# Performance work log

Hardware: AMD Instinct MI355X
Metric: run time of the kernel (lower is better)

The kernel has to match this reference:

```python
import jax, jax.numpy as jnp
import numpy as np

B, N, D, E = 16, 64, 512, 512
MSG = 512          # message_size must equal edge_feature_size (scatter into edge states)
LINK_H = 512       # GraphConv hidden channels
P = 2              # propagate_layers
HOI, ROLES = 26, 2


def setup_inputs() -> dict:
    key = jax.random.key(0)
    ks = jax.random.split(key, 12)
    s = 0.02
    return dict(
        edge_features=jax.random.normal(ks[0], (B, N, N, E), jnp.float32),
        node_features=jax.random.normal(ks[1], (B, N, D), jnp.float32),
        node_labels=jnp.zeros((B, N, HOI), jnp.float32),
        node_roles=jnp.zeros((B, N, ROLES), jnp.float32),
        # message_fun 'linear_concat_relu': Linear(D+E -> MSG) + ReLU
        Wm=(jax.random.normal(ks[2], (MSG, D + E), jnp.float32) * s),
        bm=jnp.zeros((MSG,), jnp.float32),
        # link_fun GraphConv: 1x1 Conv2d stack E->LINK_H->LINK_H->1
        Wl1=(jax.random.normal(ks[3], (LINK_H, E), jnp.float32) * s),
        bl1=jnp.zeros((LINK_H,), jnp.float32),
        Wl2=(jax.random.normal(ks[4], (LINK_H, LINK_H), jnp.float32) * s),
        bl2=jnp.zeros((LINK_H,), jnp.float32),
        Wlo=(jax.random.normal(ks[5], (1, LINK_H), jnp.float32) * s),
        blo=jnp.zeros((1,), jnp.float32),
        # update_fun GRU(input=MSG, hidden=D), torch gate order r,z,n
        W_ih=(jax.random.normal(ks[6], (3 * D, MSG), jnp.float32) * s),
        b_ih=jnp.zeros((3 * D,), jnp.float32),
        W_hh=(jax.random.normal(ks[7], (3 * D, D), jnp.float32) * s),
        b_hh=jnp.zeros((3 * D,), jnp.float32),
        # readout FCs
        Wr1=(jax.random.normal(ks[8], (HOI, D), jnp.float32) * s),
        br1=jnp.zeros((HOI,), jnp.float32),
        Wr2=(jax.random.normal(ks[9], (ROLES, D), jnp.float32) * s),
        br2=jnp.zeros((ROLES,), jnp.float32),
    )


def _link(x, Wl1, bl1, Wl2, bl2, Wlo, blo):
    # x: [B, C, N, N]; 1x1 conv stack -> [B, N, N]
    h = jax.nn.relu(jnp.einsum('bcvw,hc->bhvw', x, Wl1) + bl1[None, :, None, None])
    h = jax.nn.relu(jnp.einsum('bcvw,hc->bhvw', h, Wl2) + bl2[None, :, None, None])
    return (jnp.einsum('bcvw,hc->bhvw', h, Wlo) + blo[None, :, None, None])[:, 0]


def _forward(edge_features, node_features, Wm, bm, Wl1, bl1, Wl2, bl2, Wlo, blo,
             W_ih, b_ih, W_hh, b_hh, Wr1, br1, Wr2, br2):
    e = jnp.transpose(edge_features, (0, 3, 1, 2))   # [B,E,v,w]
    nf = jnp.transpose(node_features, (0, 2, 1))     # [B,D,N]
    # hidden node states are never written back in the source, so raw messages
    # m(h_w, e_vw) are constant across propagation rounds: compute once, vectorized over v.
    h_part = jnp.broadcast_to(nf[:, :, None, :], (B, D, N, N))   # h_w broadcast over v
    cat = jnp.concatenate([h_part, e], axis=1)                   # [B, D+E, v, w]
    M = jax.nn.relu(jnp.einsum('bcvw,mc->bmvw', cat, Wm) + bm[None, :, None, None])
    edge_state = e
    gated = M
    for _ in range(P):
        pred_adj = _link(edge_state, Wl1, bl1, Wl2, bl2, Wlo, blo)      # [B,v,w]
        gated = jax.nn.sigmoid(pred_adj)[:, None, :, :] * M            # [B,m,v,w]
        # source stores m_v into hidden_edge_states[..., :, :, i_node] (column v)
        edge_state = jnp.swapaxes(gated, 2, 3)
    m_sum = jnp.sum(gated, axis=3)                   # [B, m, v]
    x = jnp.swapaxes(m_sum, 1, 2)                    # [B, N, MSG] GRU input
    h = node_features                                # [B, N, D]  GRU hidden
    gi = x @ W_ih.T + b_ih
    gh = h @ W_hh.T + b_hh
    ir, iz, inn = jnp.split(gi, 3, axis=-1)
    hr, hz, hn = jnp.split(gh, 3, axis=-1)
    r = jax.nn.sigmoid(ir + hr)
    z = jax.nn.sigmoid(iz + hz)
    n = jnp.tanh(inn + r * hn)
    h_new = (1.0 - z) * n + z * h
    pred_node_labels = h_new @ Wr1.T + br1
    pred_node_roles = h_new @ Wr2.T + br2
    return pred_adj, pred_node_labels, pred_node_roles


def reference(edge_features, node_features, node_labels, node_roles, Wm, bm,
              Wl1, bl1, Wl2, bl2, Wlo, blo, W_ih, b_ih, W_hh, b_hh,
              Wr1, br1, Wr2, br2):
    return _forward(edge_features, node_features, Wm, bm, Wl1, bl1, Wl2, bl2,
                    Wlo, blo, W_ih, b_ih, W_hh, b_hh, Wr1, br1, Wr2, br2)
```

## Files before the change

kernel.cpp:

```cpp
#include <hip/hip_runtime.h>
#include <stdint.h>
#include <stddef.h>


using u16 = unsigned short;
using u32 = unsigned int;

__device__ __forceinline__ float u2f(u16 u) {
  union { unsigned i; float f; } c; c.i = ((unsigned)u) << 16; return c.f;
}
__device__ __forceinline__ u16 f2u(float f) {
  union { float f; unsigned i; } c; c.f = f;
  unsigned u = c.i;
  u += 0x7fffu + ((u >> 16) & 1u);
  return (u16)(u >> 16);
}
__device__ __forceinline__ u32 pk2(float lo, float hi) {
  return (u32)f2u(lo) | ((u32)f2u(hi) << 16);
}
__device__ __forceinline__ float sigm(float x) { return 1.f / (1.f + expf(-x)); }

typedef __attribute__((ext_vector_type(8))) short bfrag;
typedef __attribute__((ext_vector_type(4))) float f32x4;

__device__ __forceinline__ void gl_lds16(const u16* g, u16* l) {
  __builtin_amdgcn_global_load_lds((const __attribute__((address_space(1))) void*)g,
                                   (__attribute__((address_space(3))) void*)l,
                                   16, 0, 0);
}

#define NSEG 17
struct CvtArgs {
  const float* src[NSEG];
  u16* dst[NSEG];
  int cum[NSEG + 1];
};
__global__ __launch_bounds__(256) void cvt_multi(CvtArgs a, int total) {
  int i = blockIdx.x * 256 + threadIdx.x;
  if (i >= total) return;
  int s = 0;
  while (s + 1 < NSEG && i >= a.cum[s + 1]) ++s;
  const int off = i - a.cum[s];
  a.dst[s][off] = f2u(a.src[s][off]);
}

template <int MODE, bool A32>
__global__ __launch_bounds__(256)
void gemm_bt(const void* __restrict__ Av, int lda, size_t abase,
             const u16* __restrict__ W, int ldw, int K,
             const u16* __restrict__ bias,
             const float* __restrict__ ubuf,
             const u16* __restrict__ wlo,
             float* __restrict__ pred,
             u16* __restrict__ outb,
             float* __restrict__ outf,
             int ldc,
             const u16* __restrict__ W2, int ldw2, u16* __restrict__ outb2)
{
  __shared__ u16 smem[17408];
  constexpr int ASTR = A32 ? 72 : 64;
  u16* As = smem;
  u16* Bs = smem + (A32 ? 9216 : 8192);

  const int tid  = threadIdx.x;
  const int wave = tid >> 6, lane = tid & 63;
  const int wr = wave >> 1, wc = wave & 1;
  const int quad = lane >> 4, l16 = lane & 15;
  const int srow8 = lane >> 3;
  const int scol8 = (lane & 7) * 8;
  const int scolsw = ((lane & 7) ^ srow8) * 8;

  const int gx = gridDim.x;
  const int nwg = gx * gridDim.y;
  int flat = blockIdx.y * gx + blockIdx.x;
  if ((nwg & 7) == 0) { const int q = nwg >> 3; flat = (flat & 7) * q + (flat >> 3); }
  const int bx = flat % gx;
  const int by = flat / gx;

  const int row0 = by * 128;
  const bool isM = (MODE != 5) || (bx < 4);
  const int col0 = (MODE == 5 ? (bx & 3) : bx) * 128;
  const u16* Wp  = (MODE == 5 && !isM) ? W2  : W;
  const int ldwp = (MODE == 5 && !isM) ? ldw2 : ldw;

  f32x4 acc[4][4];
#pragma unroll
  for (int i = 0; i < 4; i++)
#pragma unroll
    for (int j = 0; j < 4; j++)
#pragma unroll
      for (int r = 0; r < 4; r++) acc[i][j][r] = 0.f;

  float4 rf[8];
  uint4  ra[4];
  if constexpr (A32) {
#pragma unroll
    for (int i = 0; i < 4; i++) {
      const int idx = i * 256 + tid, sr = idx >> 3, sc = (idx & 7) * 8;
      const float* p = (const float*)Av + (abase + (size_t)(row0 + sr)) * lda + sc;
      rf[2 * i] = *(const float4*)p;
      rf[2 * i + 1] = *(const float4*)(p + 4);
    }
#pragma unroll
    for (int i = 0; i < 4; i++) {
      ra[i].x = pk2(rf[2 * i].x, rf[2 * i].y);
      ra[i].y = pk2(rf[2 * i].z, rf[2 * i].w);
      ra[i].z = pk2(rf[2 * i + 1].x, rf[2 * i + 1].y);
      ra[i].w = pk2(rf[2 * i + 1].z, rf[2 * i + 1].w);
    }
  }

  for (int k0 = 0; k0 < K; k0 += 64) {
    __syncthreads();
    if constexpr (A32) {
#pragma unroll
      for (int i = 0; i < 4; i++) {
        const int idx = i * 256 + tid, sr = idx >> 3, sc = (idx & 7) * 8;
        *(uint4*)(As + sr * ASTR + sc) = ra[i];
      }
    } else {
#pragma unroll
      for (int i = 0; i < 4; i++) {
        const int chunk = wave * 4 + i;
        gl_lds16((const u16*)Av + (abase + (size_t)(row0 + chunk * 8 + srow8)) * lda + k0 + scolsw,
                 As + chunk * 512 + lane * 8);
      }
    }
#pragma unroll
    for (int i = 0; i < 4; i++) {
      const int chunk = wave * 4 + i;
      gl_lds16(Wp + (size_t)(col0 + chunk * 8 + srow8) * ldwp + k0 + scolsw,
               Bs + chunk * 512 + lane * 8);
    }
    __syncthreads();

    const bool more = (k0 + 64 < K);
    if constexpr (A32) {
      if (more) {
#pragma unroll
        for (int i = 0; i < 4; i++) {
          const int idx = i * 256 + tid, sr = idx >> 3, sc = (idx & 7) * 8;
          const float* p = (const float*)Av + (abase + (size_t)(row0 + sr)) * lda + (k0 + 64) + sc;
          rf[2 * i] = *(const float4*)p;
          rf[2 * i + 1] = *(const float4*)(p + 4);
        }
      }
    }

#pragma unroll
    for (int kk = 0; kk < 64; kk += 32) {
      const int cbsw = (((kk >> 3) + quad) ^ (l16 & 7)) << 3;
      bfrag af[4], bf[4];
#pragma unroll
      for (int mt = 0; mt < 4; mt++) {
        const int R = wr * 64 + mt * 16 + l16;
        if constexpr (A32)
          af[mt] = *(const bfrag*)(As + R * ASTR + kk + quad * 8);
        else
          af[mt] = *(const bfrag*)(As + R * 64 + cbsw);
      }
#pragma unroll
      for (int nt = 0; nt < 4; nt++) {
        const int R = wc * 64 + nt * 16 + l16;
        bf[nt] = *(const bfrag*)(Bs + R * 64 + cbsw);
      }
#pragma unroll
      for (int mt = 0; mt < 4; mt++)
#pragma unroll
        for (int nt = 0; nt < 4; nt++)
          acc[mt][nt] = __builtin_amdgcn_mfma_f32_16x16x32_bf16(af[mt], bf[nt], acc[mt][nt], 0, 0, 0);
    }

    if constexpr (A32) {
      if (more) {
#pragma unroll
        for (int i = 0; i < 4; i++) {
          ra[i].x = pk2(rf[2 * i].x, rf[2 * i].y);
          ra[i].y = pk2(rf[2 * i].z, rf[2 * i].w);
          ra[i].z = pk2(rf[2 * i + 1].x, rf[2 * i + 1].y);
          ra[i].w = pk2(rf[2 * i + 1].z, rf[2 * i + 1].w);
        }
      }
    }
  }

  if constexpr (MODE == 2) {
#pragma unroll
    for (int mt = 0; mt < 4; mt++) {
#pragma unroll
      for (int r = 0; r < 4; r++) {
        const int rg = row0 + wr * 64 + mt * 16 + quad * 4 + r;
        float s = 0.f;
#pragma unroll
        for (int nt = 0; nt < 4; nt++) {
          const int cg = col0 + wc * 64 + nt * 16 + l16;
          float v = acc[mt][nt][r] + u2f(bias[cg]);
          v = fmaxf(v, 0.f);
          s += v * u2f(wlo[cg]);
        }
#pragma unroll
        for (int off = 1; off < 16; off <<= 1) s += __shfl_xor(s, off, 16);
        if (l16 == 0) atomicAdd(pred + rg, s);
      }
    }
  } else if constexpr (MODE == 3) {
#pragma unroll
    for (int mt = 0; mt < 4; mt++)
#pragma unroll
      for (int nt = 0; nt < 4; nt++)
#pragma unroll
        for (int r = 0; r < 4; r++) {
          const int rg = row0 + wr * 64 + mt * 16 + quad * 4 + r;
          const int cg = col0 + wc * 64 + nt * 16 + l16;
          outf[(size_t)rg * ldc + cg] = acc[mt][nt][r] + u2f(bias[cg]);
        }
  } else {
    u16* tile = smem;
    u16* outp = (MODE == 5 && !isM) ? outb2 : outb;
    __syncthreads();
#pragma unroll
    for (int mt = 0; mt < 4; mt++)
#pragma unroll
      for (int nt = 0; nt < 4; nt++)
#pragma unroll
        for (int r = 0; r < 4; r++) {
          const int lrow = wr * 64 + mt * 16 + quad * 4 + r;
          const int lcol = wc * 64 + nt * 16 + l16;
          const int rg = row0 + lrow;
          const int cg = col0 + lcol;
          float v = acc[mt][nt][r];
          if (MODE == 0 || (MODE == 5 && isM)) {
            const size_t grow = abase + rg;
            const int urow = (int)(((grow >> 12) << 6) | (grow & 63));
            v += ubuf[(size_t)urow * 512 + cg];
            v = fmaxf(v, 0.f);
          } else if (MODE == 1 || MODE == 5) {
            v += u2f(bias[cg]);
            v = fmaxf(v, 0.f);
          } else {
            v = sigm(pred[rg]) * v + u2f(bias[cg]);
            v = fmaxf(v, 0.f);
          }
          tile[lrow * 136 + lcol] = f2u(v);
        }
    __syncthreads();
    const int row = tid >> 1, half = tid & 1;
    const u16* src = tile + row * 136 + half * 64;
    u16* dst = outp + (size_t)(row0 + row) * ldc + col0 + half * 64;
#pragma unroll
    for (int j = 0; j < 8; j++)
      *(uint4*)(dst + j * 8) = *(const uint4*)(src + j * 8);
  }
}

__global__ void fill_kernel(float* __restrict__ p, const u16* __restrict__ val, int n) {
  int i = blockIdx.x * blockDim.x + threadIdx.x;
  if (i < n) p[i] = u2f(*val);
}

__global__ void adj_out_kernel(const float* __restrict__ r, float* __restrict__ out) {
  int i = blockIdx.x * 256 + threadIdx.x;
  int b = i >> 12, v = (i >> 6) & 63, w = i & 63;
  out[i] = r[(b << 12) + (w << 6) + v];
}

__global__ __launch_bounds__(512)
void msum_kernel(const float* __restrict__ r, const u16* __restrict__ M, u16* __restrict__ x) {
  const int bv = blockIdx.x;
  const int b = bv >> 6, v = bv & 63;
  __shared__ float s[64];
  if (threadIdx.x < 64) {
    const int w = threadIdx.x;
    s[w] = sigm(r[(b << 12) + (w << 6) + v]);
  }
  __syncthreads();
  const int m = threadIdx.x;
  const u16* Mp = M + (((size_t)(b << 12) + (v << 6)) << 9) + m;
  float acc = 0.f;
#pragma unroll 8
  for (int w = 0; w < 64; w++) acc += s[w] * u2f(Mp[(size_t)w << 9]);
  x[(size_t)bv * 512 + m] = f2u(acc);
}

__global__ __launch_bounds__(256)
void gru_kernel(const float* __restrict__ gi, const float* __restrict__ gh,
                const u16* __restrict__ h, float* __restrict__ hn) {
  int i = blockIdx.x * 256 + threadIdx.x;
  int row = i >> 9, d = i & 511;
  const float* gir = gi + (size_t)row * 1536;
  const float* ghr = gh + (size_t)row * 1536;
  float rr = sigm(gir[d] + ghr[d]);
  float z  = sigm(gir[512 + d] + ghr[512 + d]);
  float n  = tanhf(gir[1024 + d] + rr * ghr[1024 + d]);
  float hv = u2f(h[i]);
  hn[i] = (1.f - z) * n + z * hv;
}

__global__ __launch_bounds__(256)
void readout_kernel(const float* __restrict__ hn,
                    const u16* __restrict__ Wr1, const u16* __restrict__ br1,
                    const u16* __restrict__ Wr2, const u16* __restrict__ br2,
                    float* __restrict__ out) {
  const int row = blockIdx.x;
  __shared__ float hrow[512];
  for (int d = threadIdx.x; d < 512; d += 256) hrow[d] = hn[(size_t)row * 512 + d];
  __syncthreads();
  const int wave = threadIdx.x >> 6, lane = threadIdx.x & 63;
  for (int j = wave; j < 28; j += 4) {
    const u16* wrow;
    float bias;
    size_t off;
    if (j < 26) { wrow = Wr1 + (size_t)j * 512; bias = u2f(br1[j]); off = 65536 + (size_t)row * 26 + j; }
    else { int jj = j - 26; wrow = Wr2 + (size_t)jj * 512; bias = u2f(br2[jj]); off = 92160 + (size_t)row * 2 + jj; }
    float s = 0.f;
    for (int d = lane; d < 512; d += 64) s += hrow[d] * u2f(wrow[d]);
#pragma unroll
    for (int o = 32; o; o >>= 1) s += __shfl_down(s, o);
    if (lane == 0) out[off] = s + bias;
  }
}

extern "C" void kernel_launch(void* const* d_in, const int* in_sizes, int n_in,
                              void* d_out, int out_size, void* d_ws, size_t ws_size,
                              hipStream_t stream)
{
  (void)in_sizes; (void)n_in; (void)out_size;
  const void*  X  = d_in[0];
  char* ws = (char*)d_ws;

  const bool big = (ws_size >= 158905344ULL);

  u16 *Mb, *H1, *xb, *nfb, *Wmb, *bmb, *Wl1b, *bl1b, *Wl2b, *bl2b, *Wlob, *blob;
  u16 *Wihb, *bihb, *Whhb, *bhhb, *Wr1b, *br1b, *Wr2b, *br2b;
  float *pred1, *rbuf, *ubuf, *gi, *gh, *hn;
  if (big) {
    Mb    = (u16*)(ws);
    H1    = (u16*)(ws + 67108864);
    pred1 = (float*)(ws + 134217728);
    rbuf  = (float*)(ws + 134479872);
    ubuf  = (float*)(ws + 134742016);
    xb    = (u16*)(ws + 136839168);
    gi    = (float*)(ws + 137887744);
    gh    = (float*)(ws + 144179200);
    hn    = (float*)(ws + 150470656);
    nfb   = (u16*)(ws + 152567808);
    Wmb   = (u16*)(ws + 153616384);
    bmb   = (u16*)(ws + 154664960);
    Wl1b  = (u16*)(ws + 154665984);
    bl1b  = (u16*)(ws + 155190272);
    Wl2b  = (u16*)(ws + 155191296);
    bl2b  = (u16*)(ws + 155715584);
    Wlob  = (u16*)(ws + 155716608);
    blob  = (u16*)(ws + 155717632);
    Wihb  = (u16*)(ws + 155718656);
    bihb  = (u16*)(ws + 157291520);
    Whhb  = (u16*)(ws + 157295616);
    bhhb  = (u16*)(ws + 158868480);
    Wr1b  = (u16*)(ws + 158872576);
    br1b  = (u16*)(ws + 158901248);
    Wr2b  = (u16*)(ws + 158902272);
    br2b  = (u16*)(ws + 158904320);
  } else {
    Mb    = (u16*)(ws);
    H1    = (u16*)(ws + 67108864);
    pred1 = (float*)(ws + 83886080);
    rbuf  = (float*)(ws + 84148224);
    ubuf  = (float*)(ws + 84410368);
    xb    = (u16*)(ws + 86507520);
    gi    = (float*)(ws + 87556096);
    gh    = (float*)(ws + 93847552);
    hn    = (float*)(ws + 100139008);
    nfb   = (u16*)(ws + 102236416);
    Wmb   = (u16*)(ws + 103284992);
    bmb   = (u16*)(ws + 104333568);
    Wl1b  = (u16*)(ws + 104334592);
    bl1b  = (u16*)(ws + 104858880);
    Wl2b  = (u16*)(ws + 104859904);
    bl2b  = (u16*)(ws + 105384192);
    Wlob  = (u16*)(ws + 105385216);
    blob  = (u16*)(ws + 105386240);
    Wihb  = (u16*)(ws + 105387264);
    bihb  = (u16*)(ws + 106960128);
    Whhb  = (u16*)(ws + 106964224);
    bhhb  = (u16*)(ws + 108537088);
    Wr1b  = (u16*)(ws + 108541184);
    br1b  = (u16*)(ws + 108573952);
    Wr2b  = (u16*)(ws + 108574976);
    br2b  = (u16*)(ws + 108579072);
  }

  float* out = (float*)d_out;

  {
    CvtArgs ca;
    const int seg_in[NSEG]  = {1,4,5,6,7,8,9,10,11,12,13,14,15,16,17,18,19};
    u16* seg_dst[NSEG] = {nfb,Wmb,bmb,Wl1b,bl1b,Wl2b,bl2b,Wlob,blob,
                          Wihb,bihb,Whhb,bhhb,Wr1b,br1b,Wr2b,br2b};
    const int seg_n[NSEG] = {524288,524288,512,262144,512,262144,512,512,1,
                             786432,1536,786432,1536,13312,26,1024,2};
    int total = 0;
    for (int s = 0; s < NSEG; s++) {
      ca.src[s] = (const float*)d_in[seg_in[s]];
      ca.dst[s] = seg_dst[s];
      ca.cum[s] = total;
      total += seg_n[s];
    }
    ca.cum[NSEG] = total;
    cvt_multi<<<(total + 255) / 256, 256, 0, stream>>>(ca, total);
  }

  gemm_bt<3, false><<<dim3(4, 8), 256, 0, stream>>>(nfb, 512, 0, Wmb, 1024, 512, bmb,
      nullptr, nullptr, nullptr, nullptr, ubuf, 512, nullptr, 0, nullptr);
  fill_kernel<<<512, 256, 0, stream>>>(pred1, blob, 131072);

  if (big) {
    gemm_bt<5, true><<<dim3(8, 512), 256, 0, stream>>>(X, 512, 0, Wmb + 512, 1024, 512,
        bl1b, ubuf, nullptr, nullptr, Mb, nullptr, 512, Wl1b, 512, H1);
    gemm_bt<2, false><<<dim3(4, 512), 256, 0, stream>>>(H1, 512, 0, Wl2b, 512, 512, bl2b,
        nullptr, Wlob, pred1, nullptr, nullptr, 512, nullptr, 0, nullptr);
    gemm_bt<4, false><<<dim3(4, 512), 256, 0, stream>>>(Mb, 512, 0, Wl1b, 512, 512, bl1b,
        nullptr, nullptr, pred1, H1, nullptr, 512, nullptr, 0, nullptr);
    gemm_bt<2, false><<<dim3(4, 512), 256, 0, stream>>>(H1, 512, 0, Wl2b, 512, 512, bl2b,
        nullptr, Wlob, rbuf, nullptr, nullptr, 512, nullptr, 0, nullptr);
  } else {
    gemm_bt<0, true><<<dim3(4, 512), 256, 0, stream>>>(X, 512, 0, Wmb + 512, 1024, 512,
        nullptr, ubuf, nullptr, nullptr, Mb, nullptr, 512, nullptr, 0, nullptr);
    for (int q = 0; q < 4; q++) {
      const size_t ro = (size_t)q * 16384;
      gemm_bt<1, true><<<dim3(4, 128), 256, 0, stream>>>(X, 512, ro, Wl1b, 512, 512, bl1b,
          nullptr, nullptr, nullptr, H1, nullptr, 512, nullptr, 0, nullptr);
      gemm_bt<2, false><<<dim3(4, 128), 256, 0, stream>>>(H1, 512, 0, Wl2b, 512, 512, bl2b,
          nullptr, Wlob, pred1 + ro, nullptr, nullptr, 512, nullptr, 0, nullptr);
    }
    for (int q = 0; q < 4; q++) {
      const size_t ro = (size_t)q * 16384;
      gemm_bt<4, false><<<dim3(4, 128), 256, 0, stream>>>(Mb, 512, ro, Wl1b, 512, 512, bl1b,
          nullptr, nullptr, pred1 + ro, H1, nullptr, 512, nullptr, 0, nullptr);
      gemm_bt<2, false><<<dim3(4, 128), 256, 0, stream>>>(H1, 512, 0, Wl2b, 512, 512, bl2b,
          nullptr, Wlob, rbuf + ro, nullptr, nullptr, 512, nullptr, 0, nullptr);
    }
  }

  adj_out_kernel<<<256, 256, 0, stream>>>(rbuf, out);
  msum_kernel<<<1024, 512, 0, stream>>>(rbuf, Mb, xb);
  gemm_bt<3, false><<<dim3(12, 8), 256, 0, stream>>>(xb, 512, 0, Wihb, 512, 512, bihb,
      nullptr, nullptr, nullptr, nullptr, gi, 1536, nullptr, 0, nullptr);
  gemm_bt<3, false><<<dim3(12, 8), 256, 0, stream>>>(nfb, 512, 0, Whhb, 512, 512, bhhb,
      nullptr, nullptr, nullptr, nullptr, gh, 1536, nullptr, 0, nullptr);
  gru_kernel<<<2048, 256, 0, stream>>>(gi, gh, nfb, hn);
  readout_kernel<<<1024, 256, 0, stream>>>(hn, Wr1b, br1b, Wr2b, br2b, out);
}
```

Baseline: 684.2 us.

## Double-buffer GEMM LDS tiles and swizzle fp32-converted A layout

Turns the bf16 GEMM main loop into a double-buffered pipeline. The next K tile is staged into a second LDS buffer while MFMAs run on the current one, which leaves one barrier per iteration instead of two. The fp32 A path now uses the same XOR-swizzled 64-wide layout instead of padded rows, and the rounding helpers use HIP bf16 intrinsics, which may map to packed conversion instructions. Shared memory doubles to 64 KB per block, which can reduce occupancy.

```diff
diff --git a/kernel.cpp b/kernel.cpp
--- a/kernel.cpp
+++ b/kernel.cpp
@@ -1,4 +1,5 @@
 #include <hip/hip_runtime.h>
+#include <hip/hip_bf16.h>
 #include <stdint.h>
 #include <stddef.h>
 
@@ -10,13 +11,12 @@
   union { unsigned i; float f; } c; c.i = ((unsigned)u) << 16; return c.f;
 }
 __device__ __forceinline__ u16 f2u(float f) {
-  union { float f; unsigned i; } c; c.f = f;
-  unsigned u = c.i;
-  u += 0x7fffu + ((u >> 16) & 1u);
-  return (u16)(u >> 16);
+  __hip_bfloat16 h = __float2bfloat16(f);
+  union { __hip_bfloat16 h; u16 u; } c; c.h = h; return c.u;
 }
 __device__ __forceinline__ u32 pk2(float lo, float hi) {
-  return (u32)f2u(lo) | ((u32)f2u(hi) << 16);
+  __hip_bfloat162 h = __float22bfloat162_rn(make_float2(lo, hi));
+  union { __hip_bfloat162 h; u32 u; } c; c.h = h; return c.u;
 }
 __device__ __forceinline__ float sigm(float x) { return 1.f / (1.f + expf(-x)); }
 
@@ -57,17 +57,15 @@
              int ldc,
              const u16* __restrict__ W2, int ldw2, u16* __restrict__ outb2)
 {
-  __shared__ u16 smem[17408];
-  constexpr int ASTR = A32 ? 72 : 64;
-  u16* As = smem;
-  u16* Bs = smem + (A32 ? 9216 : 8192);
+  __shared__ u16 smem[32768];
+  u16* const Abase = smem;
+  u16* const Bbase = smem + 16384;
 
   const int tid  = threadIdx.x;
   const int wave = tid >> 6, lane = tid & 63;
   const int wr = wave >> 1, wc = wave & 1;
   const int quad = lane >> 4, l16 = lane & 15;
   const int srow8 = lane >> 3;
-  const int scol8 = (lane & 7) * 8;
   const int scolsw = ((lane & 7) ^ srow8) * 8;
 
   const int gx = gridDim.x;
@@ -93,14 +91,33 @@
 
   float4 rf[8];
   uint4  ra[4];
-  if constexpr (A32) {
+
+  auto stageA = [&](int kk0, u16* dst) {
+#pragma unroll
+    for (int i = 0; i < 4; i++) {
+      const int chunk = wave * 4 + i;
+      gl_lds16((const u16*)Av + (abase + (size_t)(row0 + chunk * 8 + srow8)) * lda + kk0 + scolsw,
+               dst + chunk * 512 + lane * 8);
+    }
+  };
+  auto stageB = [&](int kk0, u16* dst) {
+#pragma unroll
+    for (int i = 0; i < 4; i++) {
+      const int chunk = wave * 4 + i;
+      gl_lds16(Wp + (size_t)(col0 + chunk * 8 + srow8) * ldwp + kk0 + scolsw,
+               dst + chunk * 512 + lane * 8);
+    }
+  };
+  auto loadRF = [&](int kk0) {
 #pragma unroll
     for (int i = 0; i < 4; i++) {
       const int idx = i * 256 + tid, sr = idx >> 3, sc = (idx & 7) * 8;
-      const float* p = (const float*)Av + (abase + (size_t)(row0 + sr)) * lda + sc;
-      rf[2 * i] = *(const float4*)p;
+      const float* p = (const float*)Av + (abase + (size_t)(row0 + sr)) * lda + kk0 + sc;
+      rf[2 * i]     = *(const float4*)p;
       rf[2 * i + 1] = *(const float4*)(p + 4);
     }
+  };
+  auto convRA = [&]() {
 #pragma unroll
     for (int i = 0; i < 4; i++) {
       ra[i].x = pk2(rf[2 * i].x, rf[2 * i].y);
@@ -108,80 +125,70 @@
       ra[i].z = pk2(rf[2 * i + 1].x, rf[2 * i + 1].y);
       ra[i].w = pk2(rf[2 * i + 1].z, rf[2 * i + 1].w);
     }
-  }
-
-  for (int k0 = 0; k0 < K; k0 += 64) {
-    __syncthreads();
-    if constexpr (A32) {
-#pragma unroll
-      for (int i = 0; i < 4; i++) {
-        const int idx = i * 256 + tid, sr = idx >> 3, sc = (idx & 7) * 8;
-        *(uint4*)(As + sr * ASTR + sc) = ra[i];
+  };
+  auto writeA = [&](u16* dst) {
+#pragma unroll
+    for (int i = 0; i < 4; i++) {
+      const int idx = i * 256 + tid, sr = idx >> 3, cb = idx & 7;
+      *(uint4*)(dst + sr * 64 + ((cb ^ (sr & 7)) << 3)) = ra[i];
+    }
+  };
+  auto compute = [&](const u16* Ac, const u16* Bc) {
+#pragma unroll
+    for (int kk = 0; kk < 64; kk += 32) {
+      const int cb0 = (kk >> 3) + quad;
+      const int cbsw = ((cb0 ^ (l16 & 7)) << 3);
+      bfrag af[4], bf[4];
+#pragma unroll
+      for (int mt = 0; mt < 4; mt++) {
+        const int R = wr * 64 + mt * 16 + l16;
+        af[mt] = *(const bfrag*)(Ac + R * 64 + cbsw);
       }
-    } else {
-#pragma unroll
-      for (int i = 0; i < 4; i++) {
-        const int chunk = wave * 4 + i;
-        gl_lds16((const u16*)Av + (abase + (size_t)(row0 + chunk * 8 + srow8)) * lda + k0 + scolsw,
-                 As + chunk * 512 + lane * 8);
+#pragma unroll
+      for (int nt2 = 0; nt2 < 4; nt2++) {
+        const int R = wc * 64 + nt2 * 16 + l16;
+        bf[nt2] = *(const bfrag*)(Bc + R * 64 + cbsw);
       }
-    }
-#pragma unroll
-    for (int i = 0; i < 4; i++) {
-      const int chunk = wave * 4 + i;
-      gl_lds16(Wp + (size_t)(col0 + chunk * 8 + srow8) * ldwp + k0 + scolsw,
-               Bs + chunk * 512 + lane * 8);
-    }
-    __syncthreads();
-
-    const bool more = (k0 + 64 < K);
+#pragma unroll
+      for (int mt = 0; mt < 4; mt++)
+#pragma unroll
+        for (int nt2 = 0; nt2 < 4; nt2++)
+          acc[mt][nt2] = __builtin_amdgcn_mfma_f32_16x16x32_bf16(af[mt], bf[nt2], acc[mt][nt2], 0, 0, 0);
+    }
+  };
+
+  const int ntile = K >> 6;
+  int cur = 0;
+
+  if constexpr (A32) {
+    loadRF(0); convRA(); writeA(Abase);
+    stageB(0, Bbase);
+    if (ntile > 1) loadRF(64);
+  } else {
+    stageA(0, Abase);
+    stageB(0, Bbase);
+  }
+  __syncthreads();
+
+  for (int t = 0; t < ntile; ++t) {
+    const bool more = (t + 1 < ntile);
+    u16* Ac = Abase + cur * 8192;
+    u16* Bc = Bbase + cur * 8192;
+    u16* An = Abase + (cur ^ 1) * 8192;
+    u16* Bn = Bbase + (cur ^ 1) * 8192;
+    if (more) {
+      if constexpr (!A32) stageA((t + 1) << 6, An);
+      stageB((t + 1) << 6, Bn);
+    }
+    compute(Ac, Bc);
     if constexpr (A32) {
       if (more) {
-#pragma unroll
-        for (int i = 0; i < 4; i++) {
-          const int idx = i * 256 + tid, sr = idx >> 3, sc = (idx & 7) * 8;
-          const float* p = (const float*)Av + (abase + (size_t)(row0 + sr)) * lda + (k0 + 64) + sc;
-          rf[2 * i] = *(const float4*)p;
-          rf[2 * i + 1] = *(const float4*)(p + 4);
-        }
+        convRA(); writeA(An);
+        if (t + 2 < ntile) loadRF((t + 2) << 6);
       }
     }
-
-#pragma unroll
-    for (int kk = 0; kk < 64; kk += 32) {
-      const int cbsw = (((kk >> 3) + quad) ^ (l16 & 7)) << 3;
-      bfrag af[4], bf[4];
-#pragma unroll
-      for (int mt = 0; mt < 4; mt++) {
-        const int R = wr * 64 + mt * 16 + l16;
-        if constexpr (A32)
-          af[mt] = *(const bfrag*)(As + R * ASTR + kk + quad * 8);
-        else
-          af[mt] = *(const bfrag*)(As + R * 64 + cbsw);
-      }
-#pragma unroll
-      for (int nt = 0; nt < 4; nt++) {
-        const int R = wc * 64 + nt * 16 + l16;
-        bf[nt] = *(const bfrag*)(Bs + R * 64 + cbsw);
-      }
-#pragma unroll
-      for (int mt = 0; mt < 4; mt++)
-#pragma unroll
-        for (int nt = 0; nt < 4; nt++)
-          acc[mt][nt] = __builtin_amdgcn_mfma_f32_16x16x32_bf16(af[mt], bf[nt], acc[mt][nt], 0, 0, 0);
-    }
-
-    if constexpr (A32) {
-      if (more) {
-#pragma unroll
-        for (int i = 0; i < 4; i++) {
-          ra[i].x = pk2(rf[2 * i].x, rf[2 * i].y);
-          ra[i].y = pk2(rf[2 * i].z, rf[2 * i].w);
-          ra[i].z = pk2(rf[2 * i + 1].x, rf[2 * i + 1].y);
-          ra[i].w = pk2(rf[2 * i + 1].z, rf[2 * i + 1].w);
-        }
-      }
-    }
+    __syncthreads();
+    cur ^= 1;
   }
 
   if constexpr (MODE == 2) {
```

Result: faster. 661.7 us (-3.3%).
